# Performance work log

Measured on AMD Instinct MI355X. Metric: run time of the kernel, lower is better.

Reference implementation:

```python
import jax, jax.numpy as jnp
import numpy as np

K, MU, SIGMA = 8, 0.0, 0.1
M, N, D_DIM, T = 512, 1024, 512, 4096


def setup_inputs() -> dict:
    key = jax.random.key(0)
    ks, ke, ka, kd, kl1, kl2 = jax.random.split(key, 6)
    S = jax.random.normal(ks, (N, T), dtype=jnp.float32)
    E = jax.random.normal(ke, (M, T), dtype=jnp.float32)  # raw noise; scaled by sigma/mu in reference
    A = jax.random.uniform(ka, (M, N), dtype=jnp.float32)  # torch.rand init
    Dm = jax.random.normal(kd, (N, D_DIM), dtype=jnp.float32) / jnp.sqrt(N)  # stands in for DCT-transformed randn
    c = jnp.ones((1,), dtype=jnp.float32)
    l1 = 0.1 * jnp.abs(jax.random.normal(kl1, (1,), dtype=jnp.float32)) + 0.05
    l2 = jax.random.normal(kl2, (1,), dtype=jnp.float32)
    # LISTA params per layer; all K layers get the same closed-form init in the original
    U1 = jnp.eye(D_DIM, dtype=jnp.float32) - (1.0 / c[0]) * (Dm.T @ A.T @ A @ Dm)  # [d,d]
    V1 = (1.0 / c[0]) * (Dm.T @ A.T)  # [d,m]
    U = jnp.broadcast_to(U1, (K, D_DIM, D_DIM)).copy()
    V = jnp.broadcast_to(V1, (K, D_DIM, M)).copy()
    H0 = jnp.zeros((D_DIM, T), dtype=jnp.float32)
    return {"S": S, "E": E, "A": A, "D": Dm, "U": U, "V": V, "l1": l1, "l2": l2, "c": c, "H0": H0}


def reference(S, E, A, D, U, V, l1, l2, c, H0):
    # X = A @ S + noise (E ~ randn, scaled as in torch forward)
    X = A @ S + (E * SIGMA + MU)  # [m,T]
    # Self-attention on H0 (the original loop always feeds self.H, the zero buffer,
    # into every layer -- H is never chained). Attention map = softmax((D@H0)^T (D@H0)).
    G = D @ H0                                   # [n,T]
    attn = jax.nn.softmax(G.T @ G, axis=-1)      # [T,T]
    Z = l2[0] * (H0 @ attn)                      # [d,T]
    # All K LISTA updates share the same (H0-derived) Z and X -> batch over layers.
    mat = jnp.einsum('kde,et->kdt', U, Z) + jnp.einsum('kdm,mt->kdt', V, X)  # [K,d,T]
    thres = l1[0] / c[0]
    H_all = jnp.sign(mat) * jnp.maximum(jnp.zeros((), mat.dtype), jnp.abs(mat) - thres)
    H_last = H_all[-1]                           # only the last layer's H survives the loop
    return D @ H_last                            # S_star [n,T]
```

## Files before the change

### kernel.cpp

```cpp
#include <hip/hip_runtime.h>

typedef unsigned short ushort_t;
typedef unsigned int u32;
typedef ushort_t u16x8 __attribute__((ext_vector_type(8)));
typedef ushort_t u16x4 __attribute__((ext_vector_type(4)));
typedef __bf16   bf16x8 __attribute__((ext_vector_type(8)));
typedef float    f32x4  __attribute__((ext_vector_type(4)));

#define T_DIM 4096

__device__ __forceinline__ ushort_t f2bf(float f){
  union { float f; unsigned u; } x; x.f = f;
  unsigned r = x.u + 0x7FFFu + ((x.u >> 16) & 1u);
  return (ushort_t)(r >> 16);
}

__device__ __forceinline__ void gload16(const void* g, void* l){
  __builtin_amdgcn_global_load_lds(
      (const __attribute__((address_space(1))) u32*)g,
      (__attribute__((address_space(3))) u32*)l, 16, 0, 0);
}

__global__ __launch_bounds__(256) void prep_kernel(
    const float* __restrict__ S, const float* __restrict__ A,
    const float* __restrict__ V7, const float* __restrict__ Dm,
    ushort_t* __restrict__ St, ushort_t* __restrict__ Abf,
    ushort_t* __restrict__ Vbf, ushort_t* __restrict__ Dbf)
{
  __shared__ float tile[64][65];
  const int bid = blockIdx.x, tid = threadIdx.x;
  if (bid < 1024){
    const int t0 = (bid & 63) * 64, n0 = (bid >> 6) * 64;
#pragma unroll
    for (int i = 0; i < 4; ++i){
      int g = tid + 256 * i; int row = g >> 4, cq = g & 15;
      const f32x4 v = *(const f32x4*)&S[(size_t)(n0 + row) * T_DIM + t0 + cq * 4];
#pragma unroll
      for (int j = 0; j < 4; ++j) tile[row][cq * 4 + j] = v[j];
    }
    __syncthreads();
#pragma unroll
    for (int i = 0; i < 2; ++i){
      int g = tid + 256 * i; int tl = g >> 3, nq = g & 7;
      u16x8 h;
#pragma unroll
      for (int j = 0; j < 8; ++j) h[j] = f2bf(tile[nq * 8 + j][tl]);
      *(u16x8*)&St[(size_t)(t0 + tl) * 1024 + n0 + ((nq ^ (tl & 7)) << 3)] = h;
    }
  } else {
    int pid = bid - 1024;
    const float* src; ushort_t* dst; int g, ks;
    if (pid < 256)      { src = A;  dst = Abf; g = pid * 256 + tid;        ks = 7; }
    else if (pid < 384) { src = V7; dst = Vbf; g = (pid - 256) * 256 + tid; ks = 6; }
    else                { src = Dm; dst = Dbf; g = (pid - 384) * 256 + tid; ks = 6; }
    const int r = g >> ks, cg = g & ((1 << ks) - 1);
    const int Kd = 8 << ks;
    const size_t base = (size_t)r * Kd + (size_t)cg * 8;
    const f32x4 v0 = *(const f32x4*)&src[base];
    const f32x4 v1 = *(const f32x4*)&src[base + 4];
    u16x8 h;
#pragma unroll
    for (int j = 0; j < 4; ++j){ h[j] = f2bf(v0[j]); h[j + 4] = f2bf(v1[j]); }
    *(u16x8*)&dst[(size_t)r * Kd + ((cg >> 3) << 6) + ((((cg & 7) ^ (r & 7))) << 3)] = h;
  }
}

template<int EPI, int KD>
__global__ __launch_bounds__(256) void gemm_kernel(
    const ushort_t* __restrict__ Ag, const ushort_t* __restrict__ Bg,
    void* __restrict__ Cout, const float* __restrict__ Eptr,
    const float* __restrict__ l1p, const float* __restrict__ cp)
{
  constexpr int NK = KD / 64;
  constexpr bool SWAP = (EPI != 2);
  constexpr int MF = 4;
  __shared__ __align__(16) ushort_t As[3][128 * 64];
  __shared__ __align__(16) ushort_t Bs[3][64 * 64];
  const int tid = threadIdx.x;
  const int lane = tid & 63, wid = tid >> 6;
  const int wm = wid >> 1, wn = wid & 1;
  const int lr = lane & 15, lq = lane >> 4;
  const int t0 = blockIdx.x * 128, n0 = blockIdx.y * 64;

  constexpr int P = SWAP ? 2 : MF;
  constexpr int Q = SWAP ? MF : 2;
  f32x4 acc[P][Q];
#pragma unroll
  for (int i = 0; i < P; ++i)
#pragma unroll
    for (int j = 0; j < Q; ++j) acc[i][j] = (f32x4){0.f, 0.f, 0.f, 0.f};

  auto stage = [&](int kt, int b){
#pragma unroll
    for (int i = 0; i < 4; ++i){
      int c = i * 256 + tid;
      gload16(&Ag[(size_t)(t0 + (c >> 3)) * KD + kt * 64 + (c & 7) * 8],
              &As[b][(i * 256 + (tid & 192)) * 8]);
    }
#pragma unroll
    for (int i = 0; i < 2; ++i){
      int c = i * 256 + tid;
      gload16(&Bg[(size_t)(n0 + (c >> 3)) * KD + kt * 64 + (c & 7) * 8],
              &Bs[b][(i * 256 + (tid & 192)) * 8]);
    }
  };

  auto compute = [&](int b){
#pragma unroll
    for (int ksv = 0; ksv < 2; ++ksv){
      const int kb = ksv * 4 + lq;
      bf16x8 a[MF], bb[2];
#pragma unroll
      for (int mf = 0; mf < MF; ++mf){
        int r = wm * 64 + mf * 16 + lr;
        a[mf] = *(const bf16x8*)&As[b][r * 64 + ((kb ^ (r & 7)) << 3)];
      }
#pragma unroll
      for (int nf = 0; nf < 2; ++nf){
        int r = wn * 32 + nf * 16 + lr;
        bb[nf] = *(const bf16x8*)&Bs[b][r * 64 + ((kb ^ (r & 7)) << 3)];
      }
      if constexpr (SWAP){
#pragma unroll
        for (int nf = 0; nf < 2; ++nf)
#pragma unroll
          for (int mf = 0; mf < MF; ++mf)
            acc[nf][mf] = __builtin_amdgcn_mfma_f32_16x16x32_bf16(
                bb[nf], a[mf], acc[nf][mf], 0, 0, 0);
      } else {
#pragma unroll
        for (int mf = 0; mf < MF; ++mf)
#pragma unroll
          for (int nf = 0; nf < 2; ++nf)
            acc[mf][nf] = __builtin_amdgcn_mfma_f32_16x16x32_bf16(
                a[mf], bb[nf], acc[mf][nf], 0, 0, 0);
      }
    }
  };

  stage(0, 0);
  stage(1, 1);
  for (int kt = 0; kt < NK; ++kt){
    if (kt < NK - 1) { asm volatile("s_waitcnt vmcnt(6)" ::: "memory"); }
    else             { asm volatile("s_waitcnt vmcnt(0)" ::: "memory"); }
    __builtin_amdgcn_s_barrier();
    __builtin_amdgcn_sched_barrier(0);
    if (kt + 2 < NK) stage(kt + 2, (kt + 2) % 3);
    compute(kt % 3);
  }

  if constexpr (EPI == 2){
    float* O = (float*)Cout;
#pragma unroll
    for (int mf = 0; mf < MF; ++mf)
#pragma unroll
      for (int nf = 0; nf < 2; ++nf){
        const int t = t0 + wm * 64 + mf * 16 + lq * 4;
        const int n = n0 + wn * 32 + nf * 16 + lr;
        *(f32x4*)&O[(size_t)n * T_DIM + t] = acc[mf][nf];
      }
  } else {
    const float thres = (EPI == 1) ? (l1p[0] / cp[0]) : 0.f;
    ushort_t* OT = (ushort_t*)Cout;
#pragma unroll
    for (int nf = 0; nf < 2; ++nf){
#pragma unroll
      for (int mf = 0; mf < MF; ++mf){
        const int m = n0 + wn * 32 + nf * 16 + lq * 4;
        const int t = t0 + wm * 64 + mf * 16 + lr;
        f32x4 v = acc[nf][mf];
        u16x4 h;
        if constexpr (EPI == 0){
#pragma unroll
          for (int j = 0; j < 4; ++j){
            float e = Eptr[(size_t)(m + j) * T_DIM + t];
            h[j] = f2bf(v[j] + 0.1f * e);
          }
        } else {
#pragma unroll
          for (int j = 0; j < 4; ++j){
            float av = fabsf(v[j]) - thres;
            float r = av > 0.f ? (v[j] > 0.f ? av : -av) : 0.f;
            h[j] = f2bf(r);
          }
        }
        *(u16x4*)&OT[(size_t)t * 512 + (m & ~63) +
                     (((((m >> 3) & 7) ^ (t & 7))) << 3) + (m & 7)] = h;
      }
    }
  }
}

extern "C" void kernel_launch(void* const* d_in, const int* in_sizes, int n_in,
                              void* d_out, int out_size, void* d_ws, size_t ws_size,
                              hipStream_t stream)
{
  const float* S  = (const float*)d_in[0];
  const float* E  = (const float*)d_in[1];
  const float* A  = (const float*)d_in[2];
  const float* Dm = (const float*)d_in[3];
  const float* V  = (const float*)d_in[5];
  const float* l1 = (const float*)d_in[6];
  const float* c  = (const float*)d_in[8];

  char* ws = (char*)d_ws;
  ushort_t* St  = (ushort_t*)(ws);
  ushort_t* XT  = (ushort_t*)(ws + (size_t)( 8u << 20));
  ushort_t* HT  = (ushort_t*)(ws + (size_t)(12u << 20));
  ushort_t* Abf = (ushort_t*)(ws + (size_t)(16u << 20));
  ushort_t* Vbf = (ushort_t*)(ws + (size_t)(17u << 20));
  ushort_t* Dbf = (ushort_t*)(ws + (size_t)(17u << 20) + (512u << 10));
  const float* V7 = V + (size_t)7 * 512 * 512;

  prep_kernel<<<1664, 256, 0, stream>>>(S, A, V7, Dm, St, Abf, Vbf, Dbf);
  gemm_kernel<0, 1024><<<dim3(32, 8), 256, 0, stream>>>(St, Abf, (void*)XT, E, nullptr, nullptr);
  gemm_kernel<1, 512><<<dim3(32, 8), 256, 0, stream>>>(XT, Vbf, (void*)HT, nullptr, l1, c);
  gemm_kernel<2, 512><<<dim3(32, 16), 256, 0, stream>>>(HT, Dbf, d_out, nullptr, nullptr, nullptr);
}
```

Baseline: 43.93 us.

## Split K across two wave groups per block with ping-pong staging and LDS reduction

Each GEMM block now runs 512 threads as two groups of four waves. The groups take alternating K tiles: while one group computes on a tile, the other issues global-to-LDS loads, using four LDS buffers. At the end, group 1 writes its partial accumulators to LDS and group 0 adds them and runs the epilogue. MFMA sections are also wrapped in s_setprio. The intent is more waves per block and more overlap of loads with compute on small grids (256 to 512 blocks). The cost is more LDS, a reduction step, and per-group vmcnt waits that could be fragile.

```diff
diff --git a/kernel.cpp b/kernel.cpp
--- a/kernel.cpp
+++ b/kernel.cpp
@@ -65,127 +65,159 @@
   }
 }
 
-template<int EPI, int KD>
-__global__ __launch_bounds__(256) void gemm_kernel(
+template<int EPI, int NK>
+__global__ __launch_bounds__(512, 2) void gemm_kernel(
     const ushort_t* __restrict__ Ag, const ushort_t* __restrict__ Bg,
     void* __restrict__ Cout, const float* __restrict__ Eptr,
     const float* __restrict__ l1p, const float* __restrict__ cp)
 {
-  constexpr int NK = KD / 64;
+  constexpr int KD = NK * 64;
   constexpr bool SWAP = (EPI != 2);
-  constexpr int MF = 4;
-  __shared__ __align__(16) ushort_t As[3][128 * 64];
-  __shared__ __align__(16) ushort_t Bs[3][64 * 64];
+  constexpr int P = SWAP ? 2 : 4;
+  constexpr int Q = SWAP ? 4 : 2;
+  __shared__ __align__(16) ushort_t As[4][128 * 64];
+  __shared__ __align__(16) ushort_t Bs[4][64 * 64];
   const int tid = threadIdx.x;
   const int lane = tid & 63, wid = tid >> 6;
-  const int wm = wid >> 1, wn = wid & 1;
+  const int g = wid >> 2;
+  const int s = wid & 3;
+  const int wm = s >> 1, wn = s & 1;
   const int lr = lane & 15, lq = lane >> 4;
   const int t0 = blockIdx.x * 128, n0 = blockIdx.y * 64;
-
-  constexpr int P = SWAP ? 2 : MF;
-  constexpr int Q = SWAP ? MF : 2;
+  const int ltid = tid & 255;
+
   f32x4 acc[P][Q];
 #pragma unroll
-  for (int i = 0; i < P; ++i)
-#pragma unroll
-    for (int j = 0; j < Q; ++j) acc[i][j] = (f32x4){0.f, 0.f, 0.f, 0.f};
-
-  auto stage = [&](int kt, int b){
+  for (int p = 0; p < P; ++p)
+#pragma unroll
+    for (int q = 0; q < Q; ++q) acc[p][q] = (f32x4){0.f, 0.f, 0.f, 0.f};
+
+  auto stage = [&](int kt){
+    const int slot = ((kt & 1) << 1) | ((kt >> 1) & 1);
 #pragma unroll
     for (int i = 0; i < 4; ++i){
-      int c = i * 256 + tid;
+      int c = i * 256 + ltid;
       gload16(&Ag[(size_t)(t0 + (c >> 3)) * KD + kt * 64 + (c & 7) * 8],
-              &As[b][(i * 256 + (tid & 192)) * 8]);
+              &As[slot][(i * 256 + (ltid & 192)) * 8]);
     }
 #pragma unroll
     for (int i = 0; i < 2; ++i){
-      int c = i * 256 + tid;
+      int c = i * 256 + ltid;
       gload16(&Bg[(size_t)(n0 + (c >> 3)) * KD + kt * 64 + (c & 7) * 8],
-              &Bs[b][(i * 256 + (tid & 192)) * 8]);
+              &Bs[slot][(i * 256 + (ltid & 192)) * 8]);
     }
   };
 
-  auto compute = [&](int b){
+  auto compute = [&](int kt){
+    const int slot = ((kt & 1) << 1) | ((kt >> 1) & 1);
 #pragma unroll
     for (int ksv = 0; ksv < 2; ++ksv){
       const int kb = ksv * 4 + lq;
-      bf16x8 a[MF], bb[2];
-#pragma unroll
-      for (int mf = 0; mf < MF; ++mf){
+      bf16x8 a[4], bb[2];
+#pragma unroll
+      for (int mf = 0; mf < 4; ++mf){
         int r = wm * 64 + mf * 16 + lr;
-        a[mf] = *(const bf16x8*)&As[b][r * 64 + ((kb ^ (r & 7)) << 3)];
+        a[mf] = *(const bf16x8*)&As[slot][r * 64 + ((kb ^ (r & 7)) << 3)];
       }
 #pragma unroll
       for (int nf = 0; nf < 2; ++nf){
         int r = wn * 32 + nf * 16 + lr;
-        bb[nf] = *(const bf16x8*)&Bs[b][r * 64 + ((kb ^ (r & 7)) << 3)];
-      }
+        bb[nf] = *(const bf16x8*)&Bs[slot][r * 64 + ((kb ^ (r & 7)) << 3)];
+      }
+      __builtin_amdgcn_s_setprio(1);
       if constexpr (SWAP){
 #pragma unroll
         for (int nf = 0; nf < 2; ++nf)
 #pragma unroll
-          for (int mf = 0; mf < MF; ++mf)
+          for (int mf = 0; mf < 4; ++mf)
             acc[nf][mf] = __builtin_amdgcn_mfma_f32_16x16x32_bf16(
                 bb[nf], a[mf], acc[nf][mf], 0, 0, 0);
       } else {
 #pragma unroll
-        for (int mf = 0; mf < MF; ++mf)
+        for (int mf = 0; mf < 4; ++mf)
 #pragma unroll
           for (int nf = 0; nf < 2; ++nf)
             acc[mf][nf] = __builtin_amdgcn_mfma_f32_16x16x32_bf16(
                 a[mf], bb[nf], acc[mf][nf], 0, 0, 0);
       }
+      __builtin_amdgcn_s_setprio(0);
     }
   };
 
-  stage(0, 0);
-  stage(1, 1);
+  if (g == 0){ stage(0); stage(2); }
+  else       { stage(1); }
+
   for (int kt = 0; kt < NK; ++kt){
-    if (kt < NK - 1) { asm volatile("s_waitcnt vmcnt(6)" ::: "memory"); }
-    else             { asm volatile("s_waitcnt vmcnt(0)" ::: "memory"); }
+    if ((kt & 1) == g){
+      if (kt + 2 < NK) { asm volatile("s_waitcnt vmcnt(6)" ::: "memory"); }
+      else             { asm volatile("s_waitcnt vmcnt(0)" ::: "memory"); }
+    }
     __builtin_amdgcn_s_barrier();
     __builtin_amdgcn_sched_barrier(0);
-    if (kt + 2 < NK) stage(kt + 2, (kt + 2) % 3);
-    compute(kt % 3);
-  }
-
-  if constexpr (EPI == 2){
-    float* O = (float*)Cout;
-#pragma unroll
-    for (int mf = 0; mf < MF; ++mf)
+    if ((kt & 1) == g){
+      compute(kt);
+    } else {
+      if (kt + 3 < NK) stage(kt + 3);
+    }
+  }
+
+  float* red = (float*)&As[0][0];
+  if (g == 1){
+#pragma unroll
+    for (int p = 0; p < P; ++p)
+#pragma unroll
+      for (int q = 0; q < Q; ++q)
+        *(f32x4*)&red[s * 2048 + (p * Q + q) * 256 + lane * 4] = acc[p][q];
+  }
+  asm volatile("s_waitcnt lgkmcnt(0)" ::: "memory");
+  __builtin_amdgcn_s_barrier();
+  if (g == 0){
+#pragma unroll
+    for (int p = 0; p < P; ++p)
+#pragma unroll
+      for (int q = 0; q < Q; ++q){
+        const f32x4 o = *(const f32x4*)&red[s * 2048 + (p * Q + q) * 256 + lane * 4];
+        acc[p][q] += o;
+      }
+
+    if constexpr (EPI == 2){
+      float* O = (float*)Cout;
+#pragma unroll
+      for (int mf = 0; mf < 4; ++mf)
+#pragma unroll
+        for (int nf = 0; nf < 2; ++nf){
+          const int t = t0 + wm * 64 + mf * 16 + lq * 4;
+          const int n = n0 + wn * 32 + nf * 16 + lr;
+          *(f32x4*)&O[(size_t)n * T_DIM + t] = acc[mf][nf];
+        }
+    } else {
+      const float thres = (EPI == 1) ? (l1p[0] / cp[0]) : 0.f;
+      ushort_t* OT = (ushort_t*)Cout;
 #pragma unroll
       for (int nf = 0; nf < 2; ++nf){
-        const int t = t0 + wm * 64 + mf * 16 + lq * 4;
-        const int n = n0 + wn * 32 + nf * 16 + lr;
-        *(f32x4*)&O[(size_t)n * T_DIM + t] = acc[mf][nf];
-      }
-  } else {
-    const float thres = (EPI == 1) ? (l1p[0] / cp[0]) : 0.f;
-    ushort_t* OT = (ushort_t*)Cout;
-#pragma unroll
-    for (int nf = 0; nf < 2; ++nf){
-#pragma unroll
-      for (int mf = 0; mf < MF; ++mf){
-        const int m = n0 + wn * 32 + nf * 16 + lq * 4;
-        const int t = t0 + wm * 64 + mf * 16 + lr;
-        f32x4 v = acc[nf][mf];
-        u16x4 h;
-        if constexpr (EPI == 0){
-#pragma unroll
-          for (int j = 0; j < 4; ++j){
-            float e = Eptr[(size_t)(m + j) * T_DIM + t];
-            h[j] = f2bf(v[j] + 0.1f * e);
+#pragma unroll
+        for (int mf = 0; mf < 4; ++mf){
+          const int m = n0 + wn * 32 + nf * 16 + lq * 4;
+          const int t = t0 + wm * 64 + mf * 16 + lr;
+          f32x4 v = acc[nf][mf];
+          u16x4 h;
+          if constexpr (EPI == 0){
+#pragma unroll
+            for (int j = 0; j < 4; ++j){
+              float e = Eptr[(size_t)(m + j) * T_DIM + t];
+              h[j] = f2bf(v[j] + 0.1f * e);
+            }
+          } else {
+#pragma unroll
+            for (int j = 0; j < 4; ++j){
+              float av = fabsf(v[j]) - thres;
+              float r = av > 0.f ? (v[j] > 0.f ? av : -av) : 0.f;
+              h[j] = f2bf(r);
+            }
           }
-        } else {
-#pragma unroll
-          for (int j = 0; j < 4; ++j){
-            float av = fabsf(v[j]) - thres;
-            float r = av > 0.f ? (v[j] > 0.f ? av : -av) : 0.f;
-            h[j] = f2bf(r);
-          }
+          *(u16x4*)&OT[(size_t)t * 512 + (m & ~63) +
+                       (((((m >> 3) & 7) ^ (t & 7))) << 3) + (m & 7)] = h;
         }
-        *(u16x4*)&OT[(size_t)t * 512 + (m & ~63) +
-                     (((((m >> 3) & 7) ^ (t & 7))) << 3) + (m & 7)] = h;
       }
     }
   }
@@ -213,7 +245,7 @@
   const float* V7 = V + (size_t)7 * 512 * 512;
 
   prep_kernel<<<1664, 256, 0, stream>>>(S, A, V7, Dm, St, Abf, Vbf, Dbf);
-  gemm_kernel<0, 1024><<<dim3(32, 8), 256, 0, stream>>>(St, Abf, (void*)XT, E, nullptr, nullptr);
-  gemm_kernel<1, 512><<<dim3(32, 8), 256, 0, stream>>>(XT, Vbf, (void*)HT, nullptr, l1, c);
-  gemm_kernel<2, 512><<<dim3(32, 16), 256, 0, stream>>>(HT, Dbf, d_out, nullptr, nullptr, nullptr);
-}
+  gemm_kernel<0, 16><<<dim3(32, 8), 512, 0, stream>>>(St, Abf, (void*)XT, E, nullptr, nullptr);
+  gemm_kernel<1, 8><<<dim3(32, 8), 512, 0, stream>>>(XT, Vbf, (void*)HT, nullptr, l1, c);
+  gemm_kernel<2, 8><<<dim3(32, 16), 512, 0, stream>>>(HT, Dbf, d_out, nullptr, nullptr, nullptr);
+}
```

Measured after the change: 39.38 us, median of 2. 1.12x faster.
